# Kernel tuning notes

Hardware: AMD Instinct MI355X
Metric: run time of the kernel (lower is better)

Reference implementation:

```python
import math
import jax, jax.numpy as jnp
import numpy as np

B, H, S, D = 2, 16, 2048, 1024
DK = D // H  # 64


def setup_inputs() -> dict:
    key = jax.random.key(0)
    k1, k2, k3, k4, k5 = jax.random.split(key, 5)
    scale = np.float32(0.02)
    return {
        "x": jax.random.normal(k1, (B, H, S, D), dtype=jnp.float32),
        "wq": jax.random.normal(k2, (DK, D), dtype=jnp.float32) * scale,
        "wk": jax.random.normal(k3, (DK, D), dtype=jnp.float32) * scale,
        "wv": jax.random.normal(k4, (DK, D), dtype=jnp.float32) * scale,
        "wo": jax.random.normal(k5, (D, D), dtype=jnp.float32) * scale,
    }


def reference(x, wq, wk, wv, wo):
    # x: [B, H, S, D]; wq/wk/wv: [dk, D]; wo: [D, D]
    b, h, s, d = x.shape
    xq = jnp.einsum("bhsd,kd->bhsk", x, wq)  # [B,H,S,dk]
    xk = jnp.einsum("bhsd,kd->bhsk", x, wk)
    xv = jnp.einsum("bhsd,kd->bhsk", x, wv)
    # NOTE: original scales by sqrt(hidden_dim), not sqrt(dk)
    inv_scale = np.float32(1.0 / math.sqrt(d))
    score = jnp.einsum("bhsk,bhtk->bhst", xq, xk) * inv_scale  # [B,H,S,S]
    attn = jax.nn.softmax(score, axis=-1).astype(xq.dtype)
    out = jnp.einsum("bhst,bhtk->bhsk", attn, xv)  # [B,H,S,dk]
    out = out.transpose(0, 2, 1, 3).reshape(b, s, h * (wq.shape[0]))  # [B,S,H*dk]
    return out @ wo.T  # [B,S,D]
```

## Files before the change

### kernel.cpp

```cpp
#include <hip/hip_runtime.h>
#include <math.h>

#define BB 2
#define HH 16
#define SS 2048
#define DD 1024
#define DK 64
#define BHS (BB*HH*SS)
#define QSCALE 0.04508422f

typedef short  bf16x8  __attribute__((ext_vector_type(8)));
typedef float  floatx4 __attribute__((ext_vector_type(4)));
typedef unsigned short u16;

#define MFMA(a,b,c) __builtin_amdgcn_mfma_f32_16x16x32_bf16((a),(b),(c),0,0,0)

__device__ __forceinline__ unsigned cvt_pk_bf16(float lo, float hi) {
    unsigned r;
    asm("v_cvt_pk_bf16_f32 %0, %1, %2" : "=v"(r) : "v"(lo), "v"(hi));
    return r;
}
__device__ __forceinline__ bf16x8 ldfrag(const u16* p) {
    union { uint4 u; bf16x8 b; } c;
    c.u = *(const uint4*)p;
    return c.b;
}
__device__ __forceinline__ void stbf4(u16* p, float4 t) {
    union { unsigned u[2]; uint2 v; } c;
    c.u[0] = cvt_pk_bf16(t.x, t.y);
    c.u[1] = cvt_pk_bf16(t.z, t.w);
    *(uint2*)p = c.v;
}
__device__ __forceinline__ void st4s(u16* p, float a, float b, float c, float d) {
    unsigned x = cvt_pk_bf16(a, b), y = cvt_pk_bf16(c, d);
    p[0]  = (u16)x; p[16] = (u16)(x >> 16);
    p[32] = (u16)y; p[48] = (u16)(y >> 16);
}
__device__ __forceinline__ void st2s(u16* p, float a, float b) {
    unsigned x = cvt_pk_bf16(a, b);
    p[0]  = (u16)x; p[16] = (u16)(x >> 16);
}

#define WQKV_CHUNKS (192*1024/4)
#define WO_CHUNKS   (1024*1024/4)
__global__ __launch_bounds__(256) void convert_w(
    const float* __restrict__ wq, const float* __restrict__ wk,
    const float* __restrict__ wv, const float* __restrict__ wo,
    u16* __restrict__ wqkv, u16* __restrict__ wo_bf)
{
    int i = blockIdx.x * 256 + threadIdx.x;
    if (i < WQKV_CHUNKS) {
        int r = i >> 8;
        int c = i & 255;
        const float* src = (r < 64) ? wq : ((r < 128) ? wk : wv);
        float4 t = *(const float4*)(src + (size_t)(r & 63) * DD + c * 4);
        stbf4(wqkv + (size_t)r * DD + c * 4, t);
    } else if (i < WQKV_CHUNKS + WO_CHUNKS) {
        int j = i - WQKV_CHUNKS;
        float4 t = *(const float4*)(wo + (size_t)j * 4);
        stbf4(wo_bf + (size_t)j * 4, t);
    }
}

__global__ __launch_bounds__(512) void qkv_proj(
    const float* __restrict__ x, const u16* __restrict__ wqkv,
    u16* __restrict__ q, u16* __restrict__ k, u16* __restrict__ vT)
{
    __shared__ __align__(16) u16 Ws[2][192][72];
    const int tid  = threadIdx.x;
    const int w    = tid >> 6;
    const int lane = tid & 63;
    const int quad = lane >> 4;
    const int l16  = lane & 15;
    const int rt   = w & 3;
    const int g    = w >> 2;
    const int rowbase = blockIdx.x * 64;
    const float* xr = x + (size_t)(rowbase + rt * 16 + l16) * DD + quad * 8;

    uint4 wreg[3];
    auto wload = [&](int kk) {
#pragma unroll
        for (int it = 0; it < 3; ++it) {
            int li = tid + it * 512;
            int r  = li >> 3, c8 = li & 7;
            wreg[it] = *(const uint4*)(wqkv + (size_t)r * DD + kk * 64 + c8 * 8);
        }
    };
    auto wstore = [&](int p) {
#pragma unroll
        for (int it = 0; it < 3; ++it) {
            int li = tid + it * 512;
            int r  = li >> 3, c8 = li & 7;
            *(uint4*)&Ws[p][r][c8 * 8] = wreg[it];
        }
    };

    float4 xc[4], xn[4];
    auto xload = [&](int kk, float4* d) {
        const float* p = xr + kk * 64;
        d[0] = *(const float4*)(p);
        d[1] = *(const float4*)(p + 4);
        d[2] = *(const float4*)(p + 32);
        d[3] = *(const float4*)(p + 36);
    };

    floatx4 acc[6];
#pragma unroll
    for (int j = 0; j < 6; ++j) acc[j] = (floatx4){0.f,0.f,0.f,0.f};

    wload(0); wstore(0);
    xload(0, xc);
    __syncthreads();

    for (int kk = 0; kk < 16; ++kk) {
        int p = kk & 1;
        if (kk < 15) { wload(kk + 1); xload(kk + 1, xn); }
        union { unsigned u[4]; bf16x8 v; } A0, A1;
        A0.u[0] = cvt_pk_bf16(xc[0].x, xc[0].y);
        A0.u[1] = cvt_pk_bf16(xc[0].z, xc[0].w);
        A0.u[2] = cvt_pk_bf16(xc[1].x, xc[1].y);
        A0.u[3] = cvt_pk_bf16(xc[1].z, xc[1].w);
        A1.u[0] = cvt_pk_bf16(xc[2].x, xc[2].y);
        A1.u[1] = cvt_pk_bf16(xc[2].z, xc[2].w);
        A1.u[2] = cvt_pk_bf16(xc[3].x, xc[3].y);
        A1.u[3] = cvt_pk_bf16(xc[3].z, xc[3].w);
#pragma unroll
        for (int j = 0; j < 6; ++j) {
            int n = g * 6 + j;
            bf16x8 b0 = ldfrag(&Ws[p][n * 16 + l16][quad * 8]);
            bf16x8 b1 = ldfrag(&Ws[p][n * 16 + l16][32 + quad * 8]);
            acc[j] = MFMA(A0.v, b0, acc[j]);
            acc[j] = MFMA(A1.v, b1, acc[j]);
        }
        if (kk < 15) {
            wstore(p ^ 1);
#pragma unroll
            for (int i2 = 0; i2 < 4; ++i2) xc[i2] = xn[i2];
            __syncthreads();
        }
    }

    u16 (*Vbuf)[72] = (u16 (*)[72])&Ws[0][0][0];
#pragma unroll
    for (int rr = 0; rr < 4; ++rr) {
        int rloc = rt * 16 + quad * 4 + rr;
        size_t m = (size_t)(rowbase + rloc);
        if (g == 0) {
            st4s(&q[m * DK + l16], acc[0][rr] * QSCALE, acc[1][rr] * QSCALE,
                                   acc[2][rr] * QSCALE, acc[3][rr] * QSCALE);
            st2s(&k[m * DK + l16], acc[4][rr], acc[5][rr]);
        } else {
            st2s(&k[m * DK + 32 + l16], acc[0][rr], acc[1][rr]);
            st4s(&Vbuf[rloc][l16], acc[2][rr], acc[3][rr],
                                   acc[4][rr], acc[5][rr]);
        }
    }
    __syncthreads();
    {
        const int dk = tid >> 3;
        const int sc = (tid & 7) * 8;
        const int bh = rowbase >> 11;
        const int s0 = rowbase & 2047;
        union { u16 s[8]; uint4 u; } t;
#pragma unroll
        for (int u = 0; u < 8; ++u) t.s[u] = Vbuf[sc + u][dk];
        *(uint4*)(vT + ((size_t)(bh * DK + dk)) * SS + s0 + sc) = t.u;
    }
}

__global__ __launch_bounds__(512) void flash_attn(
    const u16* __restrict__ q, const u16* __restrict__ k,
    const u16* __restrict__ vT, u16* __restrict__ ao)
{
    __shared__ __align__(16) u16 Ks[64][72];
    __shared__ __align__(16) u16 Vt[64][72];
    __shared__ __align__(16) u16 Ps[8][16][72];
    const int tid  = threadIdx.x;
    const int w    = tid >> 6;
    const int lane = tid & 63;
    const int quad = lane >> 4;
    const int l16  = lane & 15;
    const int rg   = w >> 2;
    const int rt   = w & 3;
    const int qt   = blockIdx.x;
    const int bh   = blockIdx.y;
    const size_t kbase = (size_t)bh * SS * DK;
    const size_t vbase = (size_t)bh * DK * SS;

    const u16* qrow = q + kbase +
        (size_t)(qt * 128 + rg * 64 + rt * 16 + l16) * DK;
    const bf16x8 qa0 = ldfrag(qrow + quad * 8);
    const bf16x8 qa1 = ldfrag(qrow + 32 + quad * 8);

    float m_i[4], l_i[4];
    floatx4 acc_o[4];
#pragma unroll
    for (int r = 0; r < 4; ++r) { m_i[r] = -INFINITY; l_i[r] = 0.f; }
#pragma unroll
    for (int n = 0; n < 4; ++n) acc_o[n] = (floatx4){0.f,0.f,0.f,0.f};

    for (int kt = 0; kt < SS / 64; ++kt) {
        {
            int r  = tid >> 3, c8 = tid & 7;
            *(uint4*)&Ks[r][c8 * 8] =
                *(const uint4*)(k + kbase + (size_t)(kt * 64 + r) * DK + c8 * 8);
            *(uint4*)&Vt[r][c8 * 8] =
                *(const uint4*)(vT + vbase + (size_t)r * SS + kt * 64 + c8 * 8);
        }
        __syncthreads();

        floatx4 sc[4];
        __builtin_amdgcn_s_setprio(1);
#pragma unroll
        for (int n = 0; n < 4; ++n) {
            sc[n] = (floatx4){0.f,0.f,0.f,0.f};
            bf16x8 b0 = ldfrag(&Ks[n * 16 + l16][quad * 8]);
            bf16x8 b1 = ldfrag(&Ks[n * 16 + l16][32 + quad * 8]);
            sc[n] = MFMA(qa0, b0, sc[n]);
            sc[n] = MFMA(qa1, b1, sc[n]);
        }
        __builtin_amdgcn_s_setprio(0);

        float rmx[4];
#pragma unroll
        for (int r = 0; r < 4; ++r) {
            float rm = fmaxf(fmaxf(sc[0][r], sc[1][r]), fmaxf(sc[2][r], sc[3][r]));
#pragma unroll
            for (int off = 1; off < 16; off <<= 1)
                rm = fmaxf(rm, __shfl_xor(rm, off, 64));
            rmx[r] = rm;
        }
        int ok = (rmx[0] <= m_i[0] + 8.f) & (rmx[1] <= m_i[1] + 8.f) &
                 (rmx[2] <= m_i[2] + 8.f) & (rmx[3] <= m_i[3] + 8.f);
        if (!__all(ok)) {
#pragma unroll
            for (int r = 0; r < 4; ++r) {
                float mnew  = fmaxf(m_i[r], rmx[r]);
                float alpha = __builtin_amdgcn_exp2f(m_i[r] - mnew);
#pragma unroll
                for (int n = 0; n < 4; ++n) acc_o[n][r] *= alpha;
                l_i[r] *= alpha;
                m_i[r]  = mnew;
            }
        }
#pragma unroll
        for (int r = 0; r < 4; ++r) {
            float mi = m_i[r];
            float p0 = __builtin_amdgcn_exp2f(sc[0][r] - mi);
            float p1 = __builtin_amdgcn_exp2f(sc[1][r] - mi);
            float p2 = __builtin_amdgcn_exp2f(sc[2][r] - mi);
            float p3 = __builtin_amdgcn_exp2f(sc[3][r] - mi);
            float rs = (p0 + p1) + (p2 + p3);
#pragma unroll
            for (int off = 1; off < 16; off <<= 1)
                rs += __shfl_xor(rs, off, 64);
            l_i[r] += rs;
            st4s(&Ps[w][quad * 4 + r][l16], p0, p1, p2, p3);
        }

        __builtin_amdgcn_s_setprio(1);
#pragma unroll
        for (int kc = 0; kc < 2; ++kc) {
            bf16x8 a = ldfrag(&Ps[w][l16][kc * 32 + quad * 8]);
#pragma unroll
            for (int n = 0; n < 4; ++n) {
                bf16x8 b = ldfrag(&Vt[n * 16 + l16][kc * 32 + quad * 8]);
                acc_o[n] = MFMA(a, b, acc_o[n]);
            }
        }
        __builtin_amdgcn_s_setprio(0);
        __syncthreads();
    }

    const int b = bh >> 4, h = bh & 15;
#pragma unroll
    for (int r = 0; r < 4; ++r) {
        int srow = qt * 128 + rg * 64 + rt * 16 + quad * 4 + r;
        float rl = __builtin_amdgcn_rcpf(l_i[r]);
        size_t base = ((size_t)(b * SS + srow)) * (HH * DK) + h * 64;
        st4s(&ao[base + l16], acc_o[0][r] * rl, acc_o[1][r] * rl,
                              acc_o[2][r] * rl, acc_o[3][r] * rl);
    }
}

__global__ __launch_bounds__(256) void out_proj(
    const u16* __restrict__ ao, const u16* __restrict__ wo_bf,
    float* __restrict__ out)
{
    __shared__ __align__(16) u16 As[64][72];
    __shared__ __align__(16) u16 Bs[64][72];
    const int tid  = threadIdx.x;
    const int w    = tid >> 6;
    const int lane = tid & 63;
    const int quad = lane >> 4;
    const int l16  = lane & 15;
    const int mt = blockIdx.y;
    const int nt = blockIdx.x;

    floatx4 acc[4];
#pragma unroll
    for (int n = 0; n < 4; ++n) acc[n] = (floatx4){0.f,0.f,0.f,0.f};

    for (int k0 = 0; k0 < DD; k0 += 64) {
#pragma unroll
        for (int it = 0; it < 2; ++it) {
            int li = tid + it * 256;
            int r  = li >> 3, c8 = li & 7;
            *(uint4*)&As[r][c8 * 8] =
                *(const uint4*)(ao + (size_t)(mt * 64 + r) * DD + k0 + c8 * 8);
            *(uint4*)&Bs[r][c8 * 8] =
                *(const uint4*)(wo_bf + (size_t)(nt * 64 + r) * DD + k0 + c8 * 8);
        }
        __syncthreads();

        bf16x8 a0 = ldfrag(&As[w * 16 + l16][quad * 8]);
        bf16x8 a1 = ldfrag(&As[w * 16 + l16][32 + quad * 8]);
#pragma unroll
        for (int n = 0; n < 4; ++n) {
            bf16x8 b0 = ldfrag(&Bs[n * 16 + l16][quad * 8]);
            bf16x8 b1 = ldfrag(&Bs[n * 16 + l16][32 + quad * 8]);
            acc[n] = MFMA(a0, b0, acc[n]);
            acc[n] = MFMA(a1, b1, acc[n]);
        }
        __syncthreads();
    }

#pragma unroll
    for (int r = 0; r < 4; ++r) {
        int row = mt * 64 + w * 16 + quad * 4 + r;
#pragma unroll
        for (int n = 0; n < 4; ++n)
            out[(size_t)row * DD + nt * 64 + n * 16 + l16] = acc[n][r];
    }
}

extern "C" void kernel_launch(void* const* d_in, const int* in_sizes, int n_in,
                              void* d_out, int out_size, void* d_ws, size_t ws_size,
                              hipStream_t stream) {
    const float* x  = (const float*)d_in[0];
    const float* wq = (const float*)d_in[1];
    const float* wk = (const float*)d_in[2];
    const float* wv = (const float*)d_in[3];
    const float* wo = (const float*)d_in[4];
    float* out = (float*)d_out;

    u16* q     = (u16*)d_ws;
    u16* k     = q    + (size_t)BHS * DK;
    u16* vT    = k    + (size_t)BHS * DK;
    u16* ao    = vT   + (size_t)BHS * DK;
    u16* wqkv  = ao   + (size_t)BHS * DK;
    u16* wo_bf = wqkv + (size_t)192 * DD;

    convert_w<<<dim3((WQKV_CHUNKS + WO_CHUNKS) / 256), dim3(256), 0, stream>>>(
        wq, wk, wv, wo, wqkv, wo_bf);
    qkv_proj<<<dim3(BHS / 64), dim3(512), 0, stream>>>(x, wqkv, q, k, vT);
    flash_attn<<<dim3(SS / 128, BB * HH), dim3(512), 0, stream>>>(q, k, vT, ao);
    out_proj<<<dim3(DD / 64, (BB * SS) / 64), dim3(256), 0, stream>>>(ao, wo_bf, out);
}
```

Baseline: 556.3 us.

## Stage x tiles through shared memory with coalesced loads in QKV projection

The QKV projection now loads 64x256 chunks of x with fully coalesced float4 reads, converts them to bf16 in shared memory, and feeds MFMA A-fragments from LDS. Before, each lane read strided 32-byte pieces of x directly into registers. The weight tile loses its double buffering: it is loaded and stored synchronously each k-step, which adds two barriers per step and removes the overlap of global loads with MFMA work.

```diff
diff --git a/kernel.cpp b/kernel.cpp
--- a/kernel.cpp
+++ b/kernel.cpp
@@ -66,7 +66,8 @@
     const float* __restrict__ x, const u16* __restrict__ wqkv,
     u16* __restrict__ q, u16* __restrict__ k, u16* __restrict__ vT)
 {
-    __shared__ __align__(16) u16 Ws[2][192][72];
+    __shared__ __align__(16) u16 Xq[64][264];
+    __shared__ __align__(16) u16 Ws[192][72];
     const int tid  = threadIdx.x;
     const int w    = tid >> 6;
     const int lane = tid & 63;
@@ -75,72 +76,46 @@
     const int rt   = w & 3;
     const int g    = w >> 2;
     const int rowbase = blockIdx.x * 64;
-    const float* xr = x + (size_t)(rowbase + rt * 16 + l16) * DD + quad * 8;
-
-    uint4 wreg[3];
-    auto wload = [&](int kk) {
-#pragma unroll
-        for (int it = 0; it < 3; ++it) {
+
+    floatx4 acc[6];
+#pragma unroll
+    for (int j = 0; j < 6; ++j) acc[j] = (floatx4){0.f,0.f,0.f,0.f};
+
+    for (int qd = 0; qd < 4; ++qd) {
+#pragma unroll
+        for (int it = 0; it < 8; ++it) {
             int li = tid + it * 512;
-            int r  = li >> 3, c8 = li & 7;
-            wreg[it] = *(const uint4*)(wqkv + (size_t)r * DD + kk * 64 + c8 * 8);
-        }
-    };
-    auto wstore = [&](int p) {
-#pragma unroll
-        for (int it = 0; it < 3; ++it) {
-            int li = tid + it * 512;
-            int r  = li >> 3, c8 = li & 7;
-            *(uint4*)&Ws[p][r][c8 * 8] = wreg[it];
-        }
-    };
-
-    float4 xc[4], xn[4];
-    auto xload = [&](int kk, float4* d) {
-        const float* p = xr + kk * 64;
-        d[0] = *(const float4*)(p);
-        d[1] = *(const float4*)(p + 4);
-        d[2] = *(const float4*)(p + 32);
-        d[3] = *(const float4*)(p + 36);
-    };
-
-    floatx4 acc[6];
-#pragma unroll
-    for (int j = 0; j < 6; ++j) acc[j] = (floatx4){0.f,0.f,0.f,0.f};
-
-    wload(0); wstore(0);
-    xload(0, xc);
-    __syncthreads();
-
-    for (int kk = 0; kk < 16; ++kk) {
-        int p = kk & 1;
-        if (kk < 15) { wload(kk + 1); xload(kk + 1, xn); }
-        union { unsigned u[4]; bf16x8 v; } A0, A1;
-        A0.u[0] = cvt_pk_bf16(xc[0].x, xc[0].y);
-        A0.u[1] = cvt_pk_bf16(xc[0].z, xc[0].w);
-        A0.u[2] = cvt_pk_bf16(xc[1].x, xc[1].y);
-        A0.u[3] = cvt_pk_bf16(xc[1].z, xc[1].w);
-        A1.u[0] = cvt_pk_bf16(xc[2].x, xc[2].y);
-        A1.u[1] = cvt_pk_bf16(xc[2].z, xc[2].w);
-        A1.u[2] = cvt_pk_bf16(xc[3].x, xc[3].y);
-        A1.u[3] = cvt_pk_bf16(xc[3].z, xc[3].w);
-#pragma unroll
-        for (int j = 0; j < 6; ++j) {
-            int n = g * 6 + j;
-            bf16x8 b0 = ldfrag(&Ws[p][n * 16 + l16][quad * 8]);
-            bf16x8 b1 = ldfrag(&Ws[p][n * 16 + l16][32 + quad * 8]);
-            acc[j] = MFMA(A0.v, b0, acc[j]);
-            acc[j] = MFMA(A1.v, b1, acc[j]);
-        }
-        if (kk < 15) {
-            wstore(p ^ 1);
-#pragma unroll
-            for (int i2 = 0; i2 < 4; ++i2) xc[i2] = xn[i2];
+            int r  = li >> 6, c4 = li & 63;
+            float4 t = *(const float4*)(x + (size_t)(rowbase + r) * DD
+                                          + qd * 256 + c4 * 4);
+            stbf4(&Xq[r][c4 * 4], t);
+        }
+        for (int ks = 0; ks < 4; ++ks) {
+            int kk = qd * 4 + ks;
+#pragma unroll
+            for (int it = 0; it < 3; ++it) {
+                int li = tid + it * 512;
+                int r  = li >> 3, c8 = li & 7;
+                *(uint4*)&Ws[r][c8 * 8] =
+                    *(const uint4*)(wqkv + (size_t)r * DD + kk * 64 + c8 * 8);
+            }
             __syncthreads();
-        }
-    }
-
-    u16 (*Vbuf)[72] = (u16 (*)[72])&Ws[0][0][0];
+
+            bf16x8 a0 = ldfrag(&Xq[rt * 16 + l16][ks * 64 + quad * 8]);
+            bf16x8 a1 = ldfrag(&Xq[rt * 16 + l16][ks * 64 + 32 + quad * 8]);
+#pragma unroll
+            for (int j = 0; j < 6; ++j) {
+                int n = g * 6 + j;
+                bf16x8 b0 = ldfrag(&Ws[n * 16 + l16][quad * 8]);
+                bf16x8 b1 = ldfrag(&Ws[n * 16 + l16][32 + quad * 8]);
+                acc[j] = MFMA(a0, b0, acc[j]);
+                acc[j] = MFMA(a1, b1, acc[j]);
+            }
+            __syncthreads();
+        }
+    }
+
+    u16 (*Vbuf)[72] = (u16 (*)[72])&Ws[0][0];
 #pragma unroll
     for (int rr = 0; rr < 4; ++rr) {
         int rloc = rt * 16 + quad * 4 + rr;
```

After: 526.4 us. 5.4% less time.
